# Performance work log

Hardware: AMD Instinct MI355X
Metric: run time of the kernel (lower is better)

The kernel has to match this reference:

```python
import jax, jax.numpy as jnp
import numpy as np

TEMPERATURE = 10.0  # module init temperature (training mode)


def setup_inputs() -> dict:
    key = jax.random.key(0)
    kx, kg = jax.random.split(key)
    B, C, H, W = 64, 128, 64, 64
    n = C * H * W  # 524288
    x = jax.random.normal(kx, (B, C, H, W), dtype=jnp.float32)
    # Gumbel(0,1) noise for Gumbel-top-k sampling (== multinomial w/o replacement)
    u = jax.random.uniform(kg, (B, n), dtype=jnp.float32, minval=1e-20, maxval=1.0)
    gumbel = -jnp.log(-jnp.log(u))
    k = int(round(0.1 * n))  # percent_on * n = 52429
    return {"x": x, "gumbel": gumbel, "k": k}


def reference(x, gumbel, k):
    B = x.shape[0]
    n = x.shape[1] * x.shape[2] * x.shape[3]
    flat = x.reshape(B, n)                      # [B, n]
    logits = flat / TEMPERATURE
    # Categorical sampling of k winners without replacement == top-k of
    # gumbel-perturbed logits (equivalent to softmax(logits) + multinomial).
    _, idx = jax.lax.top_k(logits + gumbel, k)  # [B, k]
    mask = jnp.zeros((B, n), dtype=x.dtype).at[jnp.arange(B)[:, None], idx].set(1.0)
    out = (flat * mask).reshape(x.shape)
    return jnp.maximum(out, 0.0)  # relu=True
```

## Files before the change

kernel.cpp:

```cpp
#include <hip/hip_runtime.h>
#include <cstdint>

#define BROWS 64
#define NCOL  524288
#define CHUNKS 32
#define CHUNK  (NCOL / CHUNKS)
#define NV4    (CHUNK / 4)
#define HBINS  4096
#define LCAP   2048
#define ECAP   1024
#define MAXCAP 24576

#define CNT_OFF  ((size_t)(1u << 20))
#define INFO_OFF ((size_t)((1u << 20) + 1024u))
#define CAND_OFF ((size_t)((1u << 20) + 8192u))

__device__ __forceinline__ uint32_t fkey(float s) {
  uint32_t b = __float_as_uint(s);
  return (b & 0x80000000u) ? ~b : (b | 0x80000000u);
}

__global__ __launch_bounds__(256) void k_zero(uint32_t* __restrict__ p, int n) {
  int i = blockIdx.x * 256 + threadIdx.x;
  if (i < n) p[i] = 0;
}

__global__ __launch_bounds__(256) void k_hist(const float* __restrict__ x,
                                              const float* __restrict__ g,
                                              uint32_t* __restrict__ hist) {
  __shared__ uint32_t h[HBINS];
  for (int i = threadIdx.x; i < HBINS; i += 256) h[i] = 0;
  __syncthreads();
  int row = blockIdx.y, chunk = blockIdx.x;
  size_t base = (size_t)row * NCOL + (size_t)chunk * CHUNK;
  const float4* x4 = (const float4*)(x + base);
  const float4* g4 = (const float4*)(g + base);
  for (int i = threadIdx.x; i < NV4; i += 256) {
    float4 a = x4[i];
    float4 b = g4[i];
    atomicAdd(&h[fkey(a.x / 10.0f + b.x) >> 20], 1u);
    atomicAdd(&h[fkey(a.y / 10.0f + b.y) >> 20], 1u);
    atomicAdd(&h[fkey(a.z / 10.0f + b.z) >> 20], 1u);
    atomicAdd(&h[fkey(a.w / 10.0f + b.w) >> 20], 1u);
  }
  __syncthreads();
  uint32_t* gh = hist + (size_t)row * HBINS;
  for (int i = threadIdx.x; i < HBINS; i += 256) {
    uint32_t v = h[i];
    if (v) atomicAdd(&gh[i], v);
  }
}

__global__ __launch_bounds__(256) void k_findbin(const uint32_t* __restrict__ hist,
                                                 const int* __restrict__ kptr,
                                                 uint32_t* __restrict__ rinfo) {
  __shared__ uint32_t h[HBINS];
  __shared__ uint32_t part[256];
  int row = blockIdx.x;
  const uint32_t* gh = hist + (size_t)row * HBINS;
  for (int i = threadIdx.x; i < HBINS; i += 256) h[i] = gh[i];
  __syncthreads();
  uint32_t s = 0;
  for (int j = 0; j < 16; ++j) s += h[threadIdx.x * 16 + j];
  part[threadIdx.x] = s;
  __syncthreads();
  if (threadIdx.x == 0) {
    uint32_t k = (uint32_t)(*kptr);
    uint32_t cum = 0;
    int seg = 255;
    for (; seg > 0; --seg) {
      if (cum + part[seg] >= k) break;
      cum += part[seg];
    }
    int bin = seg * 16 + 15;
    for (; bin > seg * 16; --bin) {
      if (cum + h[bin] >= k) break;
      cum += h[bin];
    }
    rinfo[row * 4 + 0] = (uint32_t)bin;
    rinfo[row * 4 + 1] = cum;
    rinfo[row * 4 + 2] = k - cum;
  }
}

__global__ __launch_bounds__(256) void k_select(const float* __restrict__ x,
                                                const float* __restrict__ g,
                                                const uint32_t* __restrict__ rinfo,
                                                uint64_t* __restrict__ cand,
                                                uint32_t* __restrict__ ccnt,
                                                float* __restrict__ out, int cap) {
  __shared__ uint64_t lbuf[LCAP];
  __shared__ uint32_t lcnt, lbase;
  int row = blockIdx.y, chunk = blockIdx.x;
  uint32_t selbin = rinfo[row * 4 + 0];
  if (threadIdx.x == 0) lcnt = 0;
  __syncthreads();
  size_t base = (size_t)row * NCOL + (size_t)chunk * CHUNK;
  const float4* x4 = (const float4*)(x + base);
  const float4* g4 = (const float4*)(g + base);
  float4* o4 = (float4*)(out + base);
  for (int i = threadIdx.x; i < NV4; i += 256) {
    float4 a = x4[i];
    float4 b = g4[i];
    uint32_t f0 = fkey(a.x / 10.0f + b.x);
    uint32_t f1 = fkey(a.y / 10.0f + b.y);
    uint32_t f2 = fkey(a.z / 10.0f + b.z);
    uint32_t f3 = fkey(a.w / 10.0f + b.w);
    uint32_t b0 = f0 >> 20, b1 = f1 >> 20, b2 = f2 >> 20, b3 = f3 >> 20;
    float4 o;
    o.x = (b0 > selbin) ? fmaxf(a.x, 0.0f) : 0.0f;
    o.y = (b1 > selbin) ? fmaxf(a.y, 0.0f) : 0.0f;
    o.z = (b2 > selbin) ? fmaxf(a.z, 0.0f) : 0.0f;
    o.w = (b3 > selbin) ? fmaxf(a.w, 0.0f) : 0.0f;
    o4[i] = o;
    uint32_t li = (uint32_t)(chunk * CHUNK + i * 4);
    if (b0 == selbin) { uint32_t p = atomicAdd(&lcnt, 1u); if (p < LCAP) lbuf[p] = ((uint64_t)f0 << 32) | (li + 0u); }
    if (b1 == selbin) { uint32_t p = atomicAdd(&lcnt, 1u); if (p < LCAP) lbuf[p] = ((uint64_t)f1 << 32) | (li + 1u); }
    if (b2 == selbin) { uint32_t p = atomicAdd(&lcnt, 1u); if (p < LCAP) lbuf[p] = ((uint64_t)f2 << 32) | (li + 2u); }
    if (b3 == selbin) { uint32_t p = atomicAdd(&lcnt, 1u); if (p < LCAP) lbuf[p] = ((uint64_t)f3 << 32) | (li + 3u); }
  }
  __syncthreads();
  uint32_t cnt = lcnt < LCAP ? lcnt : LCAP;
  if (threadIdx.x == 0) lbase = atomicAdd(&ccnt[row], cnt);
  __syncthreads();
  uint64_t* dst = cand + (size_t)row * (size_t)cap;
  uint32_t bse = lbase;
  for (uint32_t i = threadIdx.x; i < cnt; i += 256) {
    uint32_t p = bse + i;
    if (p < (uint32_t)cap) dst[p] = lbuf[i];
  }
}

__global__ __launch_bounds__(256) void k_finalize(const float* __restrict__ x,
                                                  const uint64_t* __restrict__ cand,
                                                  const uint32_t* __restrict__ ccnt,
                                                  const uint32_t* __restrict__ rinfo,
                                                  float* __restrict__ out, int cap) {
  __shared__ uint32_t h2[HBINS];
  __shared__ uint32_t part[256];
  __shared__ uint64_t elist[ECAP];
  __shared__ uint32_t ecnt;
  __shared__ int s_sub, s_need2;
  int row = blockIdx.x;
  uint32_t cnt = ccnt[row];
  if (cnt > (uint32_t)cap) cnt = (uint32_t)cap;
  uint32_t need = rinfo[row * 4 + 2];
  for (int i = threadIdx.x; i < HBINS; i += 256) h2[i] = 0;
  if (threadIdx.x == 0) ecnt = 0;
  __syncthreads();
  const uint64_t* c = cand + (size_t)row * (size_t)cap;
  for (uint32_t i = threadIdx.x; i < cnt; i += 256)
    atomicAdd(&h2[((uint32_t)(c[i] >> 32) >> 8) & 0xFFFu], 1u);
  __syncthreads();
  uint32_t s = 0;
  for (int j = 0; j < 16; ++j) s += h2[threadIdx.x * 16 + j];
  part[threadIdx.x] = s;
  __syncthreads();
  if (threadIdx.x == 0) {
    uint32_t cum = 0;
    int seg = 255;
    for (; seg > 0; --seg) {
      if (cum + part[seg] >= need) break;
      cum += part[seg];
    }
    int bin = seg * 16 + 15;
    for (; bin > seg * 16; --bin) {
      if (cum + h2[bin] >= need) break;
      cum += h2[bin];
    }
    s_sub = bin;
    s_need2 = (int)(need - cum);
  }
  __syncthreads();
  int sub = s_sub, need2 = s_need2;
  size_t rb = (size_t)row * NCOL;
  for (uint32_t i = threadIdx.x; i < cnt; i += 256) {
    uint64_t e = c[i];
    int mid = (int)(((uint32_t)(e >> 32) >> 8) & 0xFFFu);
    uint32_t idx = (uint32_t)e;
    if (mid > sub) {
      out[rb + idx] = fmaxf(x[rb + idx], 0.0f);
    } else if (mid == sub) {
      uint32_t p = atomicAdd(&ecnt, 1u);
      if (p < ECAP) elist[p] = e ^ 0xFFFFFFFFull;
    }
  }
  __syncthreads();
  int m = (int)(ecnt < (uint32_t)ECAP ? ecnt : (uint32_t)ECAP);
  for (int pass = 0; pass < m; ++pass) {
    for (int i = threadIdx.x; 2 * i + (pass & 1) + 1 < m; i += 256) {
      int a = 2 * i + (pass & 1);
      uint64_t va = elist[a], vb = elist[a + 1];
      if (vb > va) { elist[a] = vb; elist[a + 1] = va; }
    }
    __syncthreads();
  }
  int w = need2 < m ? need2 : m;
  for (int i = threadIdx.x; i < w; i += 256) {
    uint32_t idx = ~(uint32_t)elist[i];
    out[rb + idx] = fmaxf(x[rb + idx], 0.0f);
  }
}

extern "C" void kernel_launch(void* const* d_in, const int* in_sizes, int n_in,
                              void* d_out, int out_size, void* d_ws, size_t ws_size,
                              hipStream_t stream) {
  const float* x = (const float*)d_in[0];
  const float* g = (const float*)d_in[1];
  const int* kptr = (const int*)d_in[2];
  float* out = (float*)d_out;
  char* ws = (char*)d_ws;

  uint32_t* hist = (uint32_t*)(ws);
  uint32_t* ccnt = (uint32_t*)(ws + CNT_OFF);
  uint32_t* rinfo = (uint32_t*)(ws + INFO_OFF);
  uint64_t* cand = (uint64_t*)(ws + CAND_OFF);

  long cap_avail = ((long)ws_size - (long)CAND_OFF) / (8 * BROWS);
  int cap = cap_avail < MAXCAP ? (int)cap_avail : MAXCAP;
  if (cap < 1) cap = 1;

  int zwords = BROWS * HBINS + 64;
  k_zero<<<(zwords + 255) / 256, 256, 0, stream>>>((uint32_t*)ws, zwords);

  dim3 grid(CHUNKS, BROWS);
  k_hist<<<grid, 256, 0, stream>>>(x, g, hist);
  k_findbin<<<BROWS, 256, 0, stream>>>(hist, kptr, rinfo);
  k_select<<<grid, 256, 0, stream>>>(x, g, rinfo, cand, ccnt, out, cap);
  k_finalize<<<BROWS, 256, 0, stream>>>(x, cand, ccnt, rinfo, out, cap);
}
```

Before: 221.2 us.

## Replace full histogram pass with sampled threshold bracket estimation

Drops the full-data histogram pass and the zeroing kernel. A small per-row sample (32K of 524K elements) is used to estimate upper and lower key thresholds that bracket the k-th largest value with slack. The main pass then writes everything above the upper key, counts those elements, and collects the elements inside the bracket as candidates for an exact final selection. This removes one full read of x and g, at the cost of strided, uncoalesced sample reads and a risk of a wrong result if the true cutoff falls outside the sampled bracket or the candidate set overflows its caps.

```diff
diff --git a/kernel.cpp b/kernel.cpp
--- a/kernel.cpp
+++ b/kernel.cpp
@@ -6,99 +6,122 @@
 #define CHUNKS 32
 #define CHUNK  (NCOL / CHUNKS)
 #define NV4    (CHUNK / 4)
-#define HBINS  4096
 #define LCAP   2048
-#define ECAP   1024
+#define ECAP   512
 #define MAXCAP 24576
-
-#define CNT_OFF  ((size_t)(1u << 20))
-#define INFO_OFF ((size_t)((1u << 20) + 1024u))
-#define CAND_OFF ((size_t)((1u << 20) + 8192u))
+#define M_SAMP 32768
+#define SEGS   128
+#define SLACK  5200
+
+#define ABV_OFF   0u
+#define CCNT_OFF  256u
+#define RINFO_OFF 512u
+#define CAND_OFF  4096u
 
 __device__ __forceinline__ uint32_t fkey(float s) {
   uint32_t b = __float_as_uint(s);
   return (b & 0x80000000u) ? ~b : (b | 0x80000000u);
 }
 
-__global__ __launch_bounds__(256) void k_zero(uint32_t* __restrict__ p, int n) {
-  int i = blockIdx.x * 256 + threadIdx.x;
-  if (i < n) p[i] = 0;
-}
-
-__global__ __launch_bounds__(256) void k_hist(const float* __restrict__ x,
+__global__ __launch_bounds__(256) void k_sample(const float* __restrict__ x,
+                                                const float* __restrict__ g,
+                                                const int* __restrict__ kptr,
+                                                uint32_t* __restrict__ rinfo,
+                                                uint32_t* __restrict__ abv,
+                                                uint32_t* __restrict__ ccnt) {
+  __shared__ uint32_t hA[4][256];
+  __shared__ uint32_t hB[4][256];
+  __shared__ uint32_t bc[8];
+  int row = blockIdx.x;
+  int wid = threadIdx.x >> 6;
+  size_t rb = (size_t)row * NCOL;
+  if (threadIdx.x == 0) { abv[row] = 0; ccnt[row] = 0; }
+  for (int i = threadIdx.x; i < 1024; i += 256) {
+    ((uint32_t*)hA)[i] = 0;
+    ((uint32_t*)hB)[i] = 0;
+  }
+  __syncthreads();
+  for (int it = 0; it < M_SAMP / 256; ++it) {
+    int i = it * 256 + threadIdx.x;
+    size_t off = rb + (size_t)(i >> 8) * (NCOL / SEGS) + (i & 255);
+    uint32_t key = fkey(x[off] / 10.0f + g[off]);
+    atomicAdd(&hA[wid][key >> 24], 1u);
+  }
+  __syncthreads();
+  if (threadIdx.x == 0) {
+    uint32_t kk = (uint32_t)(*kptr);
+    uint32_t rHi = ((kk > SLACK ? kk - SLACK : 0u) / 16u) + 1u;
+    uint32_t rLo = ((kk + SLACK) / 16u) + 1u;
+    if (rLo > M_SAMP) rLo = M_SAMP;
+    uint32_t cum = 0, cumHi = 0, cumLo = 0;
+    int bHi = -1, bLo = -1;
+    for (int b = 255; b >= 0; --b) {
+      uint32_t c = hA[0][b] + hA[1][b] + hA[2][b] + hA[3][b];
+      if (bHi < 0 && cum + c >= rHi) { bHi = b; cumHi = cum; }
+      if (bLo < 0 && cum + c >= rLo) { bLo = b; cumLo = cum; }
+      cum += c;
+      if (bLo >= 0) break;
+    }
+    if (bHi < 0) bHi = 0;
+    if (bLo < 0) bLo = 0;
+    bc[0] = (uint32_t)bHi; bc[1] = rHi - cumHi;
+    bc[2] = (uint32_t)bLo; bc[3] = rLo - cumLo;
+  }
+  __syncthreads();
+  uint32_t byteHi = bc[0], byteLo = bc[2];
+  for (int i = threadIdx.x; i < 1024; i += 256) ((uint32_t*)hA)[i] = 0;
+  __syncthreads();
+  for (int it = 0; it < M_SAMP / 256; ++it) {
+    int i = it * 256 + threadIdx.x;
+    size_t off = rb + (size_t)(i >> 8) * (NCOL / SEGS) + (i & 255);
+    uint32_t key = fkey(x[off] / 10.0f + g[off]);
+    uint32_t tb = key >> 24;
+    if (tb == byteHi) atomicAdd(&hA[wid][(key >> 16) & 255u], 1u);
+    if (tb == byteLo) atomicAdd(&hB[wid][(key >> 16) & 255u], 1u);
+  }
+  __syncthreads();
+  if (threadIdx.x == 0) {
+    uint32_t rem = bc[1], cum = 0;
+    int b2 = 0;
+    for (int b = 255; b >= 0; --b) {
+      uint32_t c = hA[0][b] + hA[1][b] + hA[2][b] + hA[3][b];
+      if (cum + c >= rem) { b2 = b; break; }
+      cum += c;
+    }
+    uint32_t keyHi = (bc[0] << 24) | ((uint32_t)b2 << 16) | 0xFFFFu;
+    rem = bc[3]; cum = 0;
+    int b3 = 0;
+    for (int b = 255; b >= 0; --b) {
+      uint32_t c = hB[0][b] + hB[1][b] + hB[2][b] + hB[3][b];
+      if (cum + c >= rem) { b3 = b; break; }
+      cum += c;
+    }
+    uint32_t keyLo = (bc[2] << 24) | ((uint32_t)b3 << 16);
+    rinfo[row * 4 + 0] = keyHi;
+    rinfo[row * 4 + 1] = keyLo;
+  }
+}
+
+__global__ __launch_bounds__(256) void k_main(const float* __restrict__ x,
                                               const float* __restrict__ g,
-                                              uint32_t* __restrict__ hist) {
-  __shared__ uint32_t h[HBINS];
-  for (int i = threadIdx.x; i < HBINS; i += 256) h[i] = 0;
-  __syncthreads();
-  int row = blockIdx.y, chunk = blockIdx.x;
-  size_t base = (size_t)row * NCOL + (size_t)chunk * CHUNK;
-  const float4* x4 = (const float4*)(x + base);
-  const float4* g4 = (const float4*)(g + base);
-  for (int i = threadIdx.x; i < NV4; i += 256) {
-    float4 a = x4[i];
-    float4 b = g4[i];
-    atomicAdd(&h[fkey(a.x / 10.0f + b.x) >> 20], 1u);
-    atomicAdd(&h[fkey(a.y / 10.0f + b.y) >> 20], 1u);
-    atomicAdd(&h[fkey(a.z / 10.0f + b.z) >> 20], 1u);
-    atomicAdd(&h[fkey(a.w / 10.0f + b.w) >> 20], 1u);
-  }
-  __syncthreads();
-  uint32_t* gh = hist + (size_t)row * HBINS;
-  for (int i = threadIdx.x; i < HBINS; i += 256) {
-    uint32_t v = h[i];
-    if (v) atomicAdd(&gh[i], v);
-  }
-}
-
-__global__ __launch_bounds__(256) void k_findbin(const uint32_t* __restrict__ hist,
-                                                 const int* __restrict__ kptr,
-                                                 uint32_t* __restrict__ rinfo) {
-  __shared__ uint32_t h[HBINS];
-  __shared__ uint32_t part[256];
-  int row = blockIdx.x;
-  const uint32_t* gh = hist + (size_t)row * HBINS;
-  for (int i = threadIdx.x; i < HBINS; i += 256) h[i] = gh[i];
-  __syncthreads();
-  uint32_t s = 0;
-  for (int j = 0; j < 16; ++j) s += h[threadIdx.x * 16 + j];
-  part[threadIdx.x] = s;
-  __syncthreads();
-  if (threadIdx.x == 0) {
-    uint32_t k = (uint32_t)(*kptr);
-    uint32_t cum = 0;
-    int seg = 255;
-    for (; seg > 0; --seg) {
-      if (cum + part[seg] >= k) break;
-      cum += part[seg];
-    }
-    int bin = seg * 16 + 15;
-    for (; bin > seg * 16; --bin) {
-      if (cum + h[bin] >= k) break;
-      cum += h[bin];
-    }
-    rinfo[row * 4 + 0] = (uint32_t)bin;
-    rinfo[row * 4 + 1] = cum;
-    rinfo[row * 4 + 2] = k - cum;
-  }
-}
-
-__global__ __launch_bounds__(256) void k_select(const float* __restrict__ x,
-                                                const float* __restrict__ g,
-                                                const uint32_t* __restrict__ rinfo,
-                                                uint64_t* __restrict__ cand,
-                                                uint32_t* __restrict__ ccnt,
-                                                float* __restrict__ out, int cap) {
+                                              const uint32_t* __restrict__ rinfo,
+                                              uint64_t* __restrict__ cand,
+                                              uint32_t* __restrict__ ccnt,
+                                              uint32_t* __restrict__ abv,
+                                              float* __restrict__ out, int cap) {
   __shared__ uint64_t lbuf[LCAP];
   __shared__ uint32_t lcnt, lbase;
+  __shared__ uint32_t wsum[4];
   int row = blockIdx.y, chunk = blockIdx.x;
-  uint32_t selbin = rinfo[row * 4 + 0];
+  uint32_t keyHi = rinfo[row * 4 + 0];
+  uint32_t keyLo = rinfo[row * 4 + 1];
   if (threadIdx.x == 0) lcnt = 0;
   __syncthreads();
   size_t base = (size_t)row * NCOL + (size_t)chunk * CHUNK;
   const float4* x4 = (const float4*)(x + base);
   const float4* g4 = (const float4*)(g + base);
   float4* o4 = (float4*)(out + base);
+  uint32_t mycnt = 0;
   for (int i = threadIdx.x; i < NV4; i += 256) {
     float4 a = x4[i];
     float4 b = g4[i];
@@ -106,27 +129,32 @@
     uint32_t f1 = fkey(a.y / 10.0f + b.y);
     uint32_t f2 = fkey(a.z / 10.0f + b.z);
     uint32_t f3 = fkey(a.w / 10.0f + b.w);
-    uint32_t b0 = f0 >> 20, b1 = f1 >> 20, b2 = f2 >> 20, b3 = f3 >> 20;
     float4 o;
-    o.x = (b0 > selbin) ? fmaxf(a.x, 0.0f) : 0.0f;
-    o.y = (b1 > selbin) ? fmaxf(a.y, 0.0f) : 0.0f;
-    o.z = (b2 > selbin) ? fmaxf(a.z, 0.0f) : 0.0f;
-    o.w = (b3 > selbin) ? fmaxf(a.w, 0.0f) : 0.0f;
+    o.x = (f0 > keyHi) ? fmaxf(a.x, 0.0f) : 0.0f;
+    o.y = (f1 > keyHi) ? fmaxf(a.y, 0.0f) : 0.0f;
+    o.z = (f2 > keyHi) ? fmaxf(a.z, 0.0f) : 0.0f;
+    o.w = (f3 > keyHi) ? fmaxf(a.w, 0.0f) : 0.0f;
     o4[i] = o;
+    mycnt += (f0 > keyHi) + (f1 > keyHi) + (f2 > keyHi) + (f3 > keyHi);
     uint32_t li = (uint32_t)(chunk * CHUNK + i * 4);
-    if (b0 == selbin) { uint32_t p = atomicAdd(&lcnt, 1u); if (p < LCAP) lbuf[p] = ((uint64_t)f0 << 32) | (li + 0u); }
-    if (b1 == selbin) { uint32_t p = atomicAdd(&lcnt, 1u); if (p < LCAP) lbuf[p] = ((uint64_t)f1 << 32) | (li + 1u); }
-    if (b2 == selbin) { uint32_t p = atomicAdd(&lcnt, 1u); if (p < LCAP) lbuf[p] = ((uint64_t)f2 << 32) | (li + 2u); }
-    if (b3 == selbin) { uint32_t p = atomicAdd(&lcnt, 1u); if (p < LCAP) lbuf[p] = ((uint64_t)f3 << 32) | (li + 3u); }
-  }
-  __syncthreads();
-  uint32_t cnt = lcnt < LCAP ? lcnt : LCAP;
-  if (threadIdx.x == 0) lbase = atomicAdd(&ccnt[row], cnt);
-  __syncthreads();
+    if (f0 >= keyLo && f0 <= keyHi) { uint32_t p = atomicAdd(&lcnt, 1u); if (p < LCAP) lbuf[p] = ((uint64_t)f0 << 32) | li; }
+    if (f1 >= keyLo && f1 <= keyHi) { uint32_t p = atomicAdd(&lcnt, 1u); if (p < LCAP) lbuf[p] = ((uint64_t)f1 << 32) | (li + 1u); }
+    if (f2 >= keyLo && f2 <= keyHi) { uint32_t p = atomicAdd(&lcnt, 1u); if (p < LCAP) lbuf[p] = ((uint64_t)f2 << 32) | (li + 2u); }
+    if (f3 >= keyLo && f3 <= keyHi) { uint32_t p = atomicAdd(&lcnt, 1u); if (p < LCAP) lbuf[p] = ((uint64_t)f3 << 32) | (li + 3u); }
+  }
+  for (int off = 32; off > 0; off >>= 1) mycnt += __shfl_down(mycnt, off);
+  int lane = threadIdx.x & 63, wid = threadIdx.x >> 6;
+  if (lane == 0) wsum[wid] = mycnt;
+  __syncthreads();
+  if (threadIdx.x == 0) {
+    atomicAdd(&abv[row], wsum[0] + wsum[1] + wsum[2] + wsum[3]);
+    lbase = atomicAdd(&ccnt[row], lcnt < LCAP ? lcnt : (uint32_t)LCAP);
+  }
+  __syncthreads();
+  uint32_t cnt = lcnt < LCAP ? lcnt : (uint32_t)LCAP;
   uint64_t* dst = cand + (size_t)row * (size_t)cap;
-  uint32_t bse = lbase;
   for (uint32_t i = threadIdx.x; i < cnt; i += 256) {
-    uint32_t p = bse + i;
+    uint32_t p = lbase + i;
     if (p < (uint32_t)cap) dst[p] = lbuf[i];
   }
 }
@@ -134,68 +162,84 @@
 __global__ __launch_bounds__(256) void k_finalize(const float* __restrict__ x,
                                                   const uint64_t* __restrict__ cand,
                                                   const uint32_t* __restrict__ ccnt,
+                                                  const uint32_t* __restrict__ abv,
                                                   const uint32_t* __restrict__ rinfo,
+                                                  const int* __restrict__ kptr,
                                                   float* __restrict__ out, int cap) {
-  __shared__ uint32_t h2[HBINS];
+  __shared__ uint32_t h[4096];
   __shared__ uint32_t part[256];
   __shared__ uint64_t elist[ECAP];
   __shared__ uint32_t ecnt;
-  __shared__ int s_sub, s_need2;
+  __shared__ int s_cut, s_need2;
   int row = blockIdx.x;
-  uint32_t cnt = ccnt[row];
-  if (cnt > (uint32_t)cap) cnt = (uint32_t)cap;
-  uint32_t need = rinfo[row * 4 + 2];
-  for (int i = threadIdx.x; i < HBINS; i += 256) h2[i] = 0;
+  uint32_t m = ccnt[row];
+  if (m > (uint32_t)cap) m = (uint32_t)cap;
+  int need = (int)((uint32_t)(*kptr)) - (int)abv[row];
+  if (need <= 0) return;
+  size_t rb = (size_t)row * NCOL;
+  const uint64_t* c = cand + (size_t)row * (size_t)cap;
+  if ((uint32_t)need >= m) {
+    for (uint32_t i = threadIdx.x; i < m; i += 256) {
+      uint32_t idx = (uint32_t)c[i];
+      out[rb + idx] = fmaxf(x[rb + idx], 0.0f);
+    }
+    return;
+  }
+  uint32_t keyLo = rinfo[row * 4 + 1];
+  uint32_t range = rinfo[row * 4 + 0] - keyLo;
+  int bits = 32 - __clz((int)(range | 1u));
+  int shift = bits > 12 ? bits - 12 : 0;
+  for (int i = threadIdx.x; i < 4096; i += 256) h[i] = 0;
   if (threadIdx.x == 0) ecnt = 0;
   __syncthreads();
-  const uint64_t* c = cand + (size_t)row * (size_t)cap;
-  for (uint32_t i = threadIdx.x; i < cnt; i += 256)
-    atomicAdd(&h2[((uint32_t)(c[i] >> 32) >> 8) & 0xFFFu], 1u);
+  for (uint32_t i = threadIdx.x; i < m; i += 256) {
+    uint32_t key = (uint32_t)(c[i] >> 32);
+    atomicAdd(&h[(key - keyLo) >> shift], 1u);
+  }
   __syncthreads();
   uint32_t s = 0;
-  for (int j = 0; j < 16; ++j) s += h2[threadIdx.x * 16 + j];
+  for (int j = 0; j < 16; ++j) s += h[threadIdx.x * 16 + j];
   part[threadIdx.x] = s;
   __syncthreads();
   if (threadIdx.x == 0) {
     uint32_t cum = 0;
     int seg = 255;
     for (; seg > 0; --seg) {
-      if (cum + part[seg] >= need) break;
+      if (cum + part[seg] >= (uint32_t)need) break;
       cum += part[seg];
     }
     int bin = seg * 16 + 15;
     for (; bin > seg * 16; --bin) {
-      if (cum + h2[bin] >= need) break;
-      cum += h2[bin];
-    }
-    s_sub = bin;
-    s_need2 = (int)(need - cum);
-  }
-  __syncthreads();
-  int sub = s_sub, need2 = s_need2;
-  size_t rb = (size_t)row * NCOL;
-  for (uint32_t i = threadIdx.x; i < cnt; i += 256) {
+      if (cum + h[bin] >= (uint32_t)need) break;
+      cum += h[bin];
+    }
+    s_cut = bin;
+    s_need2 = need - (int)cum;
+  }
+  __syncthreads();
+  int cut = s_cut, need2 = s_need2;
+  for (uint32_t i = threadIdx.x; i < m; i += 256) {
     uint64_t e = c[i];
-    int mid = (int)(((uint32_t)(e >> 32) >> 8) & 0xFFFu);
-    uint32_t idx = (uint32_t)e;
-    if (mid > sub) {
+    int bin = (int)(((uint32_t)(e >> 32) - keyLo) >> shift);
+    if (bin > cut) {
+      uint32_t idx = (uint32_t)e;
       out[rb + idx] = fmaxf(x[rb + idx], 0.0f);
-    } else if (mid == sub) {
+    } else if (bin == cut) {
       uint32_t p = atomicAdd(&ecnt, 1u);
       if (p < ECAP) elist[p] = e ^ 0xFFFFFFFFull;
     }
   }
   __syncthreads();
-  int m = (int)(ecnt < (uint32_t)ECAP ? ecnt : (uint32_t)ECAP);
-  for (int pass = 0; pass < m; ++pass) {
-    for (int i = threadIdx.x; 2 * i + (pass & 1) + 1 < m; i += 256) {
-      int a = 2 * i + (pass & 1);
-      uint64_t va = elist[a], vb = elist[a + 1];
-      if (vb > va) { elist[a] = vb; elist[a + 1] = va; }
+  int mm = (int)(ecnt < (uint32_t)ECAP ? ecnt : (uint32_t)ECAP);
+  for (int pass = 0; pass < mm; ++pass) {
+    for (int i = threadIdx.x; 2 * i + (pass & 1) + 1 < mm; i += 256) {
+      int a2 = 2 * i + (pass & 1);
+      uint64_t va = elist[a2], vb = elist[a2 + 1];
+      if (vb > va) { elist[a2] = vb; elist[a2 + 1] = va; }
     }
     __syncthreads();
   }
-  int w = need2 < m ? need2 : m;
+  int w = need2 < mm ? need2 : mm;
   for (int i = threadIdx.x; i < w; i += 256) {
     uint32_t idx = ~(uint32_t)elist[i];
     out[rb + idx] = fmaxf(x[rb + idx], 0.0f);
@@ -211,21 +255,17 @@
   float* out = (float*)d_out;
   char* ws = (char*)d_ws;
 
-  uint32_t* hist = (uint32_t*)(ws);
-  uint32_t* ccnt = (uint32_t*)(ws + CNT_OFF);
-  uint32_t* rinfo = (uint32_t*)(ws + INFO_OFF);
+  uint32_t* abv = (uint32_t*)(ws + ABV_OFF);
+  uint32_t* ccnt = (uint32_t*)(ws + CCNT_OFF);
+  uint32_t* rinfo = (uint32_t*)(ws + RINFO_OFF);
   uint64_t* cand = (uint64_t*)(ws + CAND_OFF);
 
   long cap_avail = ((long)ws_size - (long)CAND_OFF) / (8 * BROWS);
   int cap = cap_avail < MAXCAP ? (int)cap_avail : MAXCAP;
   if (cap < 1) cap = 1;
 
-  int zwords = BROWS * HBINS + 64;
-  k_zero<<<(zwords + 255) / 256, 256, 0, stream>>>((uint32_t*)ws, zwords);
-
+  k_sample<<<BROWS, 256, 0, stream>>>(x, g, kptr, rinfo, abv, ccnt);
   dim3 grid(CHUNKS, BROWS);
-  k_hist<<<grid, 256, 0, stream>>>(x, g, hist);
-  k_findbin<<<BROWS, 256, 0, stream>>>(hist, kptr, rinfo);
-  k_select<<<grid, 256, 0, stream>>>(x, g, rinfo, cand, ccnt, out, cap);
-  k_finalize<<<BROWS, 256, 0, stream>>>(x, cand, ccnt, rinfo, out, cap);
-}
+  k_main<<<grid, 256, 0, stream>>>(x, g, rinfo, cand, ccnt, abv, out, cap);
+  k_finalize<<<BROWS, 256, 0, stream>>>(x, cand, ccnt, abv, rinfo, kptr, out, cap);
+}
```

After: 270.1 us. 1.22x slower.
